# Performance work log

Measured on AMD Instinct MI355X. Metric: run time of the kernel, lower is better.

## Reference

```python
import jax, jax.numpy as jnp
import numpy as np
from jax import lax

KERNEL = 2
STACKS = 2
LAYERS = 10
DILATIONS = [2 ** l for _ in range(STACKS) for l in range(LAYERS)]  # 20 blocks
RECEPTIVE_FIELD = sum((KERNEL - 1) * d for d in DILATIONS)  # 2046


def setup_inputs() -> dict:
    key = jax.random.key(0)
    ks = jax.random.split(key, 8)
    B, L, C, NC = 8, 4096, 256, 256
    NB = len(DILATIONS)
    SK = L - RECEPTIVE_FIELD  # 2050

    def rn(k, shape, scale):
        return jax.random.normal(k, shape, jnp.float32) * scale

    return {
        "input_x": jax.random.normal(ks[0], (B, L, 1), jnp.float32),
        "causal_w": rn(ks[1], (1, C), 1.0),                 # 1x1 causal conv, in=1
        "causal_b": jnp.zeros((C,), jnp.float32),
        "dil_w": rn(ks[2], (NB, KERNEL, C, C), (KERNEL * C) ** -0.5),  # WIO per block
        "dil_b": jnp.zeros((NB, C), jnp.float32),
        "res_w": rn(ks[3], (NB, C, C), C ** -0.5),
        "res_b": jnp.zeros((NB, C), jnp.float32),
        "skip_w": rn(ks[4], (NB, C, C), C ** -0.5),
        "skip_b": jnp.zeros((NB, C), jnp.float32),
        "cls_conv_w": rn(ks[5], (C, C), C ** -0.5),
        "cls_conv_b": jnp.zeros((C,), jnp.float32),
        "dense_w": rn(ks[6], (SK * C, NC), (SK * C) ** -0.5),
        "dense_b": jnp.zeros((NC,), jnp.float32),
    }


def _conv1x1(x, w, b):
    # x: [B, T, Cin], w: [Cin, Cout]
    return jnp.einsum("btc,co->bto", x, w) + b


def _dilated_causal_conv(x, w, b, d):
    # keras 'causal' pad followed by slicing off the first (k-1)*d frames
    # is exactly a VALID dilated conv. x: [B,T,Cin], w: [K,Cin,Cout]
    y = lax.conv_general_dilated(
        x, w, window_strides=(1,), padding="VALID", rhs_dilation=(d,),
        dimension_numbers=("NWC", "WIO", "NWC"))
    return y + b


def reference(input_x, causal_w, causal_b, dil_w, dil_b, res_w, res_b,
              skip_w, skip_b, cls_conv_w, cls_conv_b, dense_w, dense_b):
    # initial causal conv (kernel_size=1 -> plain 1x1 conv)
    x = _conv1x1(input_x, causal_w, causal_b)  # [B, L, C]
    skip_size = x.shape[1] - RECEPTIVE_FIELD

    skips = []
    for i, d in enumerate(DILATIONS):
        h = _dilated_causal_conv(x, dil_w[i], dil_b[i], d)  # [B, T-(k-1)d, C]
        g = jnp.tanh(h) * jax.nn.sigmoid(h)                  # gated activation
        res = _conv1x1(g, res_w[i], res_b[i])
        x = res + g                                          # residual (same length)
        s = _conv1x1(g, skip_w[i], skip_b[i])[:, -skip_size:]
        skips.append(s)

    # classifier head: mean over blocks, relu, shared 1x1 conv twice, dense+softmax
    s = jnp.mean(jnp.stack(skips, 0), axis=0)  # [B, skip_size, C]
    s = jax.nn.relu(s)
    s = _conv1x1(s, cls_conv_w, cls_conv_b)
    s = jax.nn.relu(s)
    s = _conv1x1(s, cls_conv_w, cls_conv_b)    # same conv applied twice (shared weights)
    f = s.reshape(s.shape[0], -1)              # flatten [B, skip_size*C]
    logits = f @ dense_w + dense_b
    return jax.nn.softmax(logits, axis=-1)
```

## Files before the change

kernel.cpp:

```cpp
#include <hip/hip_runtime.h>

typedef __attribute__((ext_vector_type(8))) short short8;
typedef __attribute__((ext_vector_type(4))) float f32x4;
typedef unsigned int uint32;
typedef unsigned short u16;

#define CCH   256
#define BATCH 8
#define LFULL 4096
#define SKL   2050
#define BM    128
#define BN    128
#define LDK   72

#define GSTRIDE ((size_t)BATCH * LFULL * CCH)
#define XSTR    ((size_t)LFULL * CCH)
#define SSTR    ((size_t)SKL * CCH)
#define PSTR    ((size_t)BATCH * SKL * CCH)

__device__ const int TOUT[20] = {4095,4093,4089,4081,4065,4033,3969,3841,3585,3073,
                                 3072,3070,3066,3058,3042,3010,2946,2818,2562,2050};

__device__ __forceinline__ u16 f2b(float f) {
  uint32 u = __float_as_uint(f);
  u += 0x7fff + ((u >> 16) & 1);
  return (u16)(u >> 16);
}
__device__ __forceinline__ float gatef(float h) {
  float hc = fmaxf(h, -30.0f);
  float q = __expf(-hc);
  return (1.0f - q) * __builtin_amdgcn_rcpf(fmaf(q, q, 1.0f));
}
__device__ __forceinline__ void glds16(const void* g, void* l) {
  __builtin_amdgcn_global_load_lds(
      (const __attribute__((address_space(1))) void*)g,
      (__attribute__((address_space(3))) void*)l, 16, 0, 0);
}
__device__ __forceinline__ int xcd_swz(int orig, int nwg) {
  int xcd = orig & 7, idx = orig >> 3;
  int q = nwg >> 3, r = nwg & 7;
  int base = (xcd < r) ? xcd * (q + 1) : r * (q + 1) + (xcd - r) * q;
  return base + idx;
}

__global__ __launch_bounds__(256)
void compose_w(const float* __restrict__ res_w, const float* __restrict__ dil_w,
               u16* __restrict__ DWc) {
  __shared__ float As[32][256];
  int bx = blockIdx.x;
  int chunk = bx & 7, tap = (bx >> 3) & 1, bi = bx >> 4;
  int i = bi + 1;
  int co = threadIdx.x;
  int ci0 = chunk * 32;

  for (int idx = threadIdx.x; idx < 32 * 256; idx += 256) {
    int r = idx >> 8, m = idx & 255;
    float v = res_w[((size_t)(bi * 256 + ci0 + r)) * 256 + m];
    if (ci0 + r == m) v += 1.0f;
    As[r][m] = v;
  }
  __syncthreads();

  float acc[32];
  #pragma unroll
  for (int r = 0; r < 32; ++r) acc[r] = 0.0f;

  const float* Wb = dil_w + ((size_t)(i * 2 + tap) * 256) * 256 + co;
  for (int m4 = 0; m4 < 64; ++m4) {
    const float* wp = Wb + (size_t)m4 * 4 * 256;
    float w0 = wp[0], w1 = wp[256], w2 = wp[512], w3 = wp[768];
    #pragma unroll
    for (int r = 0; r < 32; ++r) {
      float4 a = *(const float4*)&As[r][m4 * 4];
      acc[r] = fmaf(a.x, w0, acc[r]);
      acc[r] = fmaf(a.y, w1, acc[r]);
      acc[r] = fmaf(a.z, w2, acc[r]);
      acc[r] = fmaf(a.w, w3, acc[r]);
    }
  }
  u16* op = DWc + ((size_t)(bi * 256 + co)) * 512 + tap * 256 + ci0;
  #pragma unroll
  for (int r = 0; r < 32; ++r) op[r] = f2b(acc[r]);
}

__global__ __launch_bounds__(256)
void compose_bias(const float* __restrict__ res_b, const float* __restrict__ dil_w,
                  const float* __restrict__ dil_b, float* __restrict__ Bc) {
  int bi = blockIdx.x, i = bi + 1, co = threadIdx.x;
  float acc = dil_b[(size_t)i * 256 + co];
  const float* W0 = dil_w + ((size_t)(i * 2 + 0) * 256) * 256;
  const float* W1 = dil_w + ((size_t)(i * 2 + 1) * 256) * 256;
  for (int m = 0; m < 256; ++m) {
    float rb = res_b[(size_t)bi * 256 + m];
    acc = fmaf(rb, W0[(size_t)m * 256 + co] + W1[(size_t)m * 256 + co], acc);
  }
  Bc[(size_t)bi * 256 + co] = acc;
}

__global__ __launch_bounds__(256)
void head0(const float* __restrict__ causal_w, const float* __restrict__ causal_b,
           const float* __restrict__ dil_w, const float* __restrict__ dil_b,
           float* __restrict__ U) {
  int co = threadIdx.x;
  float u0 = 0.f, u1 = 0.f, b0 = dil_b[co];
  for (int m = 0; m < 256; ++m) {
    float cwm = causal_w[m], cbm = causal_b[m];
    float w0 = dil_w[(size_t)m * 256 + co];
    float w1 = dil_w[(size_t)(256 + m) * 256 + co];
    u0 = fmaf(cwm, w0, u0);
    u1 = fmaf(cwm, w1, u1);
    b0 = fmaf(cbm, w0 + w1, b0);
  }
  U[co] = u0; U[256 + co] = u1; U[512 + co] = b0;
}

__global__ __launch_bounds__(256)
void g0_init(const float* __restrict__ in, const float* __restrict__ U,
             u16* __restrict__ G0) {
  int t = blockIdx.x, b = blockIdx.y, co = threadIdx.x;
  float x0 = in[(size_t)b * LFULL + t];
  float x1 = in[(size_t)b * LFULL + t + 1];
  float h = fmaf(x0, U[co], fmaf(x1, U[256 + co], U[512 + co]));
  G0[((size_t)b * LFULL + t) * CCH + co] = f2b(gatef(h));
}

__global__ __launch_bounds__(256)
void pack_skipT(const float* __restrict__ w, u16* __restrict__ o) {
  int e = blockIdx.x * 256 + threadIdx.x;
  int co = e & 255, ci = (e >> 8) & 255, i = e >> 16;
  o[(size_t)co * 5120 + i * 256 + ci] = f2b(w[e]);
}
__global__ __launch_bounds__(256)
void pack_cls(const float* __restrict__ w, u16* __restrict__ o) {
  int e = blockIdx.x * 256 + threadIdx.x;
  int co = e & 255, ci = e >> 8;
  o[(size_t)co * 256 + ci] = f2b(w[e]);
}
__global__ __launch_bounds__(256)
void sbsum_k(const float* __restrict__ sb, float* __restrict__ o) {
  int n = threadIdx.x;
  float s = 0.f;
  for (int i = 0; i < 20; ++i) s += sb[(size_t)i * 256 + n];
  o[n] = s;
}

__global__ __launch_bounds__(256)
void gatem(const u16* __restrict__ Ain, int d, int Tout, int ntile,
           const u16* __restrict__ Wt, const float* __restrict__ bias,
           u16* __restrict__ Gout) {
  __shared__ u16 As[2][BM * 64];
  __shared__ u16 Bs[2][BN * 64];

  const int tid = threadIdx.x;
  const int nwg = ntile * 16;
  const int wgid = xcd_swz(blockIdx.x, nwg);
  const int tx = wgid % ntile;
  const int rem = wgid / ntile;
  const int ny = rem & 1;
  const int bb = rem >> 1;

  const int t0 = tx * BM;
  const int n0 = ny * BN;
  const int lane = tid & 63, wv = tid >> 6;
  const int wm = wv >> 1, wn = wv & 1;
  const int fr = lane & 15, fq = lane >> 4;
  const int rl = lane >> 3;
  const int subx = ((lane & 7) ^ rl) * 8;
  const int rowb = wv * 32;

  const u16* Ab = Ain + (size_t)bb * XSTR;

  f32x4 acc[4][4];
  #pragma unroll
  for (int fn = 0; fn < 4; ++fn) {
    float4 bv = *(const float4*)&bias[n0 + wn * 64 + fn * 16 + fq * 4];
    #pragma unroll
    for (int fm = 0; fm < 4; ++fm) acc[fm][fn] = (f32x4){bv.x, bv.y, bv.z, bv.w};
  }

  auto STAGE = [&](int kt, int sel) {
    const int tap = kt >> 2, ks0 = (kt & 3) * 64;
    #pragma unroll
    for (int qq = 0; qq < 4; ++qq) {
      int rr = rowb + qq * 8 + rl;
      int t = t0 + rr;
      if (t > Tout - 1) t = Tout - 1;
      glds16(Ab + (size_t)(t + tap * d) * CCH + ks0 + subx,
             &As[sel][(rowb + qq * 8) * 64]);
      glds16(Wt + (size_t)(n0 + rr) * 512 + kt * 64 + subx,
             &Bs[sel][(rowb + qq * 8) * 64]);
    }
  };

  STAGE(0, 0);
  for (int kt = 0; kt < 8; ++kt) {
    const int cur = kt & 1;
    if (kt < 7) {
      STAGE(kt + 1, cur ^ 1);
      asm volatile("s_waitcnt vmcnt(8)" ::: "memory");
    } else {
      asm volatile("s_waitcnt vmcnt(0)" ::: "memory");
    }
    __builtin_amdgcn_s_barrier();
    __builtin_amdgcn_sched_barrier(0);

    #pragma unroll
    for (int ks = 0; ks < 2; ++ks) {
      short8 af[4], bfr[4];
      #pragma unroll
      for (int fm = 0; fm < 4; ++fm) {
        int row = wm * 64 + fm * 16 + fr;
        af[fm] = *(const short8*)&As[cur][row * 64 + ((ks * 4 + fq) ^ (row & 7)) * 8];
      }
      #pragma unroll
      for (int fn = 0; fn < 4; ++fn) {
        int row = wn * 64 + fn * 16 + fr;
        bfr[fn] = *(const short8*)&Bs[cur][row * 64 + ((ks * 4 + fq) ^ (row & 7)) * 8];
      }
      #pragma unroll
      for (int fm = 0; fm < 4; ++fm)
        #pragma unroll
        for (int fn = 0; fn < 4; ++fn)
          acc[fm][fn] = __builtin_amdgcn_mfma_f32_16x16x32_bf16(
              bfr[fn], af[fm], acc[fm][fn], 0, 0, 0);
    }
    __builtin_amdgcn_s_barrier();
  }

  u16* Ob = Gout + (size_t)bb * XSTR;
  #pragma unroll
  for (int fm = 0; fm < 4; ++fm) {
    int t = t0 + wm * 64 + fm * 16 + fr;
    if (t >= Tout) continue;
    #pragma unroll
    for (int fn = 0; fn < 4; ++fn) {
      int c0 = n0 + wn * 64 + fn * 16 + fq * 4;
      f32x4 a = acc[fm][fn];
      uint32 p0 = (uint32)f2b(gatef(a[0])) | ((uint32)f2b(gatef(a[1])) << 16);
      uint32 p1 = (uint32)f2b(gatef(a[2])) | ((uint32)f2b(gatef(a[3])) << 16);
      uint2 pk; pk.x = p0; pk.y = p1;
      *(uint2*)(Ob + (size_t)t * CCH + c0) = pk;
    }
  }
}

__global__ __launch_bounds__(256)
void skipm(const u16* __restrict__ Gh, const u16* __restrict__ SWT,
           float* __restrict__ P) {
  __shared__ u16 As[2][BM * 64];
  __shared__ u16 Bs[2][BN * 64];

  const int tid = threadIdx.x;
  const int nwg = 17 * 2 * 32;
  const int wgid = xcd_swz(blockIdx.x, nwg);
  const int tx = wgid % 17;
  const int rem = wgid / 17;
  const int ny = rem & 1;
  const int zz = rem >> 1;
  const int b = zz >> 2, j = zz & 3;

  const int t0 = tx * BM;
  const int n0 = ny * BN;
  const int lane = tid & 63, wv = tid >> 6;
  const int wm = wv >> 1, wn = wv & 1;
  const int fr = lane & 15, fq = lane >> 4;
  const int rl = lane >> 3;
  const int subx = ((lane & 7) ^ rl) * 8;
  const int rowb = wv * 32;

  f32x4 acc[4][4];
  #pragma unroll
  for (int fm = 0; fm < 4; ++fm)
    #pragma unroll
    for (int fn = 0; fn < 4; ++fn) acc[fm][fn] = (f32x4){0.f, 0.f, 0.f, 0.f};

  auto STAGE = [&](int kt, int sel) {
    const int i = j * 5 + (kt >> 2);
    const int toff = TOUT[i] - SKL;
    const int ks0 = (kt & 3) * 64;
    const u16* Gi = Gh + (size_t)i * GSTRIDE + (size_t)b * XSTR;
    #pragma unroll
    for (int qq = 0; qq < 4; ++qq) {
      int rr = rowb + qq * 8 + rl;
      int t = t0 + rr;
      if (t > SKL - 1) t = SKL - 1;
      glds16(Gi + (size_t)(toff + t) * CCH + ks0 + subx,
             &As[sel][(rowb + qq * 8) * 64]);
      glds16(SWT + (size_t)(n0 + rr) * 5120 + i * 256 + ks0 + subx,
             &Bs[sel][(rowb + qq * 8) * 64]);
    }
  };

  STAGE(0, 0);
  for (int kt = 0; kt < 20; ++kt) {
    const int cur = kt & 1;
    if (kt < 19) {
      STAGE(kt + 1, cur ^ 1);
      asm volatile("s_waitcnt vmcnt(8)" ::: "memory");
    } else {
      asm volatile("s_waitcnt vmcnt(0)" ::: "memory");
    }
    __builtin_amdgcn_s_barrier();
    __builtin_amdgcn_sched_barrier(0);

    #pragma unroll
    for (int ks = 0; ks < 2; ++ks) {
      short8 af[4], bfr[4];
      #pragma unroll
      for (int fm = 0; fm < 4; ++fm) {
        int row = wm * 64 + fm * 16 + fr;
        af[fm] = *(const short8*)&As[cur][row * 64 + ((ks * 4 + fq) ^ (row & 7)) * 8];
      }
      #pragma unroll
      for (int fn = 0; fn < 4; ++fn) {
        int row = wn * 64 + fn * 16 + fr;
        bfr[fn] = *(const short8*)&Bs[cur][row * 64 + ((ks * 4 + fq) ^ (row & 7)) * 8];
      }
      #pragma unroll
      for (int fm = 0; fm < 4; ++fm)
        #pragma unroll
        for (int fn = 0; fn < 4; ++fn)
          acc[fm][fn] = __builtin_amdgcn_mfma_f32_16x16x32_bf16(
              bfr[fn], af[fm], acc[fm][fn], 0, 0, 0);
    }
    __builtin_amdgcn_s_barrier();
  }

  float* Pj = P + (size_t)j * PSTR + (size_t)b * SSTR;
  #pragma unroll
  for (int fm = 0; fm < 4; ++fm) {
    int t = t0 + wm * 64 + fm * 16 + fr;
    if (t >= SKL) continue;
    #pragma unroll
    for (int fn = 0; fn < 4; ++fn) {
      int c0 = n0 + wn * 64 + fn * 16 + fq * 4;
      f32x4 a = acc[fm][fn];
      float4 o = {a[0], a[1], a[2], a[3]};
      *(float4*)(Pj + (size_t)t * CCH + c0) = o;
    }
  }
}

enum { MODE_CLS1 = 1, MODE_CLS2 = 2 };

template <int MODE>
__global__ __launch_bounds__(256)
void convm(const void* __restrict__ Ainv, long a_bstride,
           const u16* __restrict__ Wt, const float* __restrict__ bias,
           const float* __restrict__ extra,
           void* __restrict__ Out1, long out_bstride, int Tout) {
  __shared__ u16 As[BM * LDK];
  __shared__ u16 Bs[BN * LDK];

  const int tid = threadIdx.x;
  const int bb  = blockIdx.z;
  const int t0  = blockIdx.x * BM;
  const int n0  = blockIdx.y * BN;
  const int lane = tid & 63, wv = tid >> 6;
  const int wm = wv >> 1, wn = wv & 1;
  const int fr = lane & 15, fq = lane >> 4;

  f32x4 acc[4][4];
  #pragma unroll
  for (int fn = 0; fn < 4; ++fn) {
    float bv = bias[n0 + wn * 64 + fn * 16 + fr];
    #pragma unroll
    for (int fm = 0; fm < 4; ++fm) acc[fm][fn] = (f32x4){bv, bv, bv, bv};
  }

  for (int kt = 0; kt < 4; ++kt) {
    for (int idx = tid; idx < 1024; idx += 256) {
      int r = idx >> 3, c8 = idx & 7;
      int t = t0 + r; if (t > Tout - 1) t = Tout - 1;
      uint4 v;
      if constexpr (MODE == MODE_CLS1) {
        const float* p0 = (const float*)Ainv + (size_t)bb * a_bstride +
                          (size_t)t * CCH + kt * 64 + c8 * 8;
        float4 s0 = *(const float4*)p0;
        float4 s1 = *(const float4*)(p0 + 4);
        #pragma unroll
        for (int jj = 1; jj < 4; ++jj) {
          const float* pj = p0 + (size_t)jj * PSTR;
          float4 a0 = *(const float4*)pj;
          float4 a1 = *(const float4*)(pj + 4);
          s0.x += a0.x; s0.y += a0.y; s0.z += a0.z; s0.w += a0.w;
          s1.x += a1.x; s1.y += a1.y; s1.z += a1.z; s1.w += a1.w;
        }
        float4 e0 = *(const float4*)&extra[kt * 64 + c8 * 8];
        float4 e1 = *(const float4*)&extra[kt * 64 + c8 * 8 + 4];
        u16 tmp[8];
        tmp[0] = f2b(fmaxf((s0.x + e0.x) * 0.05f, 0.f));
        tmp[1] = f2b(fmaxf((s0.y + e0.y) * 0.05f, 0.f));
        tmp[2] = f2b(fmaxf((s0.z + e0.z) * 0.05f, 0.f));
        tmp[3] = f2b(fmaxf((s0.w + e0.w) * 0.05f, 0.f));
        tmp[4] = f2b(fmaxf((s1.x + e1.x) * 0.05f, 0.f));
        tmp[5] = f2b(fmaxf((s1.y + e1.y) * 0.05f, 0.f));
        tmp[6] = f2b(fmaxf((s1.z + e1.z) * 0.05f, 0.f));
        tmp[7] = f2b(fmaxf((s1.w + e1.w) * 0.05f, 0.f));
        v = *(uint4*)tmp;
      } else {
        const u16* sp = (const u16*)Ainv + (size_t)bb * a_bstride +
                        (size_t)t * CCH + kt * 64 + c8 * 8;
        uint4 raw = *(const uint4*)sp;
        u16 tmp[8];
        *(uint4*)tmp = raw;
        #pragma unroll
        for (int jj = 0; jj < 8; ++jj) tmp[jj] = (tmp[jj] & 0x8000) ? (u16)0 : tmp[jj];
        v = *(uint4*)tmp;
      }
      *(uint4*)&As[r * LDK + c8 * 8] = v;
    }
    for (int idx = tid; idx < 1024; idx += 256) {
      int r = idx >> 3, c8 = idx & 7;
      const u16* sp = Wt + (size_t)(n0 + r) * 256 + kt * 64 + c8 * 8;
      *(uint4*)&Bs[r * LDK + c8 * 8] = *(const uint4*)sp;
    }
    __syncthreads();

    #pragma unroll
    for (int ks = 0; ks < 2; ++ks) {
      short8 af[4], bfr[4];
      #pragma unroll
      for (int fm = 0; fm < 4; ++fm)
        af[fm] = *(const short8*)&As[(wm * 64 + fm * 16 + fr) * LDK + ks * 32 + fq * 8];
      #pragma unroll
      for (int fn = 0; fn < 4; ++fn)
        bfr[fn] = *(const short8*)&Bs[(wn * 64 + fn * 16 + fr) * LDK + ks * 32 + fq * 8];
      #pragma unroll
      for (int fm = 0; fm < 4; ++fm)
        #pragma unroll
        for (int fn = 0; fn < 4; ++fn)
          acc[fm][fn] = __builtin_amdgcn_mfma_f32_16x16x32_bf16(
              af[fm], bfr[fn], acc[fm][fn], 0, 0, 0);
    }
    __syncthreads();
  }

  #pragma unroll
  for (int fm = 0; fm < 4; ++fm) {
    int rbase = t0 + wm * 64 + fm * 16 + fq * 4;
    #pragma unroll
    for (int r = 0; r < 4; ++r) {
      int t = rbase + r;
      if (t >= Tout) continue;
      #pragma unroll
      for (int fn = 0; fn < 4; ++fn) {
        int c = n0 + wn * 64 + fn * 16 + fr;
        float a = acc[fm][fn][r];
        size_t oix = (size_t)bb * out_bstride + (size_t)t * CCH + c;
        if constexpr (MODE == MODE_CLS1) {
          ((u16*)Out1)[oix] = f2b(a);
        } else {
          ((float*)Out1)[oix] = a;
        }
      }
    }
  }
}

__global__ __launch_bounds__(256)
void dense_partial(const float* __restrict__ f, const float* __restrict__ W,
                   float* __restrict__ part) {
  int tstep = blockIdx.x;
  int n = threadIdx.x;
  __shared__ float fs[BATCH][CCH];
  for (int idx = threadIdx.x; idx < BATCH * CCH; idx += 256) {
    int b = idx >> 8, c = idx & 255;
    fs[b][c] = f[((size_t)b * SKL + tstep) * CCH + c];
  }
  __syncthreads();
  float acc[BATCH] = {0.f, 0.f, 0.f, 0.f, 0.f, 0.f, 0.f, 0.f};
  const float* Wr = W + (size_t)tstep * CCH * CCH;
  for (int ci = 0; ci < CCH; ++ci) {
    float w = Wr[(size_t)ci * CCH + n];
    #pragma unroll
    for (int b = 0; b < BATCH; ++b) acc[b] = fmaf(fs[b][ci], w, acc[b]);
  }
  #pragma unroll
  for (int b = 0; b < BATCH; ++b)
    part[((size_t)tstep * BATCH + b) * CCH + n] = acc[b];
}

__global__ __launch_bounds__(256)
void reduce_part(const float* __restrict__ part, float* __restrict__ part2) {
  int chunk = blockIdx.x, b = blockIdx.y, n = threadIdx.x;
  int c0 = chunk * 33;
  int c1 = c0 + 33; if (c1 > SKL) c1 = SKL;
  float s = 0.f;
  for (int c = c0; c < c1; ++c) s += part[((size_t)c * BATCH + b) * CCH + n];
  part2[((size_t)b * 64 + chunk) * CCH + n] = s;
}

__global__ __launch_bounds__(256)
void softmax_k(const float* __restrict__ part2, const float* __restrict__ db,
               float* __restrict__ out) {
  int b = blockIdx.x, n = threadIdx.x;
  float s = db[n];
  for (int ch = 0; ch < 64; ++ch) s += part2[((size_t)b * 64 + ch) * CCH + n];

  __shared__ float r4[4];
  __shared__ float mglob, sglob;
  int wid = n >> 6, lane = n & 63;

  float m = s;
  #pragma unroll
  for (int off = 1; off < 64; off <<= 1) m = fmaxf(m, __shfl_xor(m, off));
  if (lane == 0) r4[wid] = m;
  __syncthreads();
  if (n == 0) mglob = fmaxf(fmaxf(r4[0], r4[1]), fmaxf(r4[2], r4[3]));
  __syncthreads();

  float e = expf(s - mglob);
  float se = e;
  #pragma unroll
  for (int off = 1; off < 64; off <<= 1) se += __shfl_xor(se, off);
  if (lane == 0) r4[wid] = se;
  __syncthreads();
  if (n == 0) sglob = r4[0] + r4[1] + r4[2] + r4[3];
  __syncthreads();

  out[(size_t)b * CCH + n] = e / sglob;
}

extern "C" void kernel_launch(void* const* d_in, const int* in_sizes, int n_in,
                              void* d_out, int out_size, void* d_ws, size_t ws_size,
                              hipStream_t stream) {
  const float* input_x  = (const float*)d_in[0];
  const float* causal_w = (const float*)d_in[1];
  const float* causal_b = (const float*)d_in[2];
  const float* dil_w    = (const float*)d_in[3];
  const float* dil_b    = (const float*)d_in[4];
  const float* res_w    = (const float*)d_in[5];
  const float* res_b    = (const float*)d_in[6];
  const float* skip_w   = (const float*)d_in[7];
  const float* skip_b   = (const float*)d_in[8];
  const float* cls_w    = (const float*)d_in[9];
  const float* cls_b    = (const float*)d_in[10];
  const float* dense_w  = (const float*)d_in[11];
  const float* dense_b  = (const float*)d_in[12];
  float* out = (float*)d_out;

  char* p = (char*)d_ws;
  u16*   Gh    = (u16*)p;   p += GSTRIDE * 20 * 2;
  float* P     = (float*)p; p += PSTR * 4 * 4;
  u16*   S1    = (u16*)p;   p += (size_t)BATCH * SKL * CCH * 2;
  float* S2    = (float*)p; p += (size_t)BATCH * SKL * CCH * 4;
  float* PART  = (float*)p; p += (size_t)SKL * BATCH * CCH * 4;
  float* PART2 = (float*)p; p += (size_t)BATCH * 64 * CCH * 4;
  u16*   DWc   = (u16*)p;   p += (size_t)19 * 256 * 512 * 2;
  float* Bc    = (float*)p; p += (size_t)19 * 256 * 4;
  u16*   SWT   = (u16*)p;   p += (size_t)256 * 5120 * 2;
  u16*   CW    = (u16*)p;   p += (size_t)256 * 256 * 2;
  float* U     = (float*)p; p += (size_t)768 * 4;
  float* SBS   = (float*)p; p += (size_t)256 * 4;

  static const int dil[20] = {1, 2, 4, 8, 16, 32, 64, 128, 256, 512,
                              1, 2, 4, 8, 16, 32, 64, 128, 256, 512};
  static const int tout_h[20] = {4095,4093,4089,4081,4065,4033,3969,3841,3585,3073,
                                 3072,3070,3066,3058,3042,3010,2946,2818,2562,2050};
  dim3 blk(256);
  const int stile = (SKL + BM - 1) / BM;

  compose_w   <<<dim3(19 * 2 * 8), blk, 0, stream>>>(res_w, dil_w, DWc);
  compose_bias<<<dim3(19), blk, 0, stream>>>(res_b, dil_w, dil_b, Bc);
  head0       <<<dim3(1), blk, 0, stream>>>(causal_w, causal_b, dil_w, dil_b, U);
  pack_skipT  <<<dim3(20 * 256), blk, 0, stream>>>(skip_w, SWT);
  pack_cls    <<<dim3(256), blk, 0, stream>>>(cls_w, CW);
  sbsum_k     <<<dim3(1), blk, 0, stream>>>(skip_b, SBS);

  g0_init<<<dim3(4095, BATCH), blk, 0, stream>>>(input_x, U, Gh);

  for (int i = 1; i < 20; ++i) {
    int Tout = tout_h[i];
    int ntile = (Tout + BM - 1) / BM;
    gatem<<<dim3(ntile * 16), blk, 0, stream>>>(
        Gh + (size_t)(i - 1) * GSTRIDE, dil[i], Tout, ntile,
        DWc + (size_t)(i - 1) * 256 * 512, Bc + (size_t)(i - 1) * 256,
        Gh + (size_t)i * GSTRIDE);
  }

  skipm<<<dim3(17 * 2 * 32), blk, 0, stream>>>(Gh, SWT, P);

  convm<MODE_CLS1><<<dim3(stile, 2, BATCH), blk, 0, stream>>>(
      P, (long)SSTR, CW, cls_b, SBS, S1, (long)SSTR, SKL);
  convm<MODE_CLS2><<<dim3(stile, 2, BATCH), blk, 0, stream>>>(
      S1, (long)SSTR, CW, cls_b, nullptr, S2, (long)SSTR, SKL);

  dense_partial<<<dim3(SKL), blk, 0, stream>>>(S2, dense_w, PART);
  reduce_part<<<dim3(64, BATCH), blk, 0, stream>>>(PART, PART2);
  softmax_k<<<dim3(BATCH), blk, 0, stream>>>(PART2, dense_b, out);
}
```

Baseline: 703.8 us.

## Load weight fragments directly into registers instead of staging through LDS

In both the gated dilated-conv GEMM and the skip GEMM, the B (weight) operand is no longer staged in shared memory. Each wave loads its weight fragments from global memory straight into double-buffered registers, and the k-loop is fully unrolled. This halves LDS use and removes LDS reads for B, which may raise occupancy. The cost is extra VGPRs, redundant global weight loads across the wave-rows that share B (relying on cache), and a waitcnt count that must match the new load count.

```diff
diff --git a/kernel.cpp b/kernel.cpp
--- a/kernel.cpp
+++ b/kernel.cpp
@@ -149,7 +149,6 @@
            const u16* __restrict__ Wt, const float* __restrict__ bias,
            u16* __restrict__ Gout) {
   __shared__ u16 As[2][BM * 64];
-  __shared__ u16 Bs[2][BN * 64];
 
   const int tid = threadIdx.x;
   const int nwg = ntile * 16;
@@ -169,6 +168,7 @@
   const int rowb = wv * 32;
 
   const u16* Ab = Ain + (size_t)bb * XSTR;
+  const u16* Wb = Wt + (size_t)(n0 + wn * 64 + fr) * 512 + fq * 8;
 
   f32x4 acc[4][4];
   #pragma unroll
@@ -178,7 +178,7 @@
     for (int fm = 0; fm < 4; ++fm) acc[fm][fn] = (f32x4){bv.x, bv.y, bv.z, bv.w};
   }
 
-  auto STAGE = [&](int kt, int sel) {
+  auto STAGE_A = [&](int kt, int sel) {
     const int tap = kt >> 2, ks0 = (kt & 3) * 64;
     #pragma unroll
     for (int qq = 0; qq < 4; ++qq) {
@@ -187,17 +187,29 @@
       if (t > Tout - 1) t = Tout - 1;
       glds16(Ab + (size_t)(t + tap * d) * CCH + ks0 + subx,
              &As[sel][(rowb + qq * 8) * 64]);
-      glds16(Wt + (size_t)(n0 + rr) * 512 + kt * 64 + subx,
-             &Bs[sel][(rowb + qq * 8) * 64]);
     }
   };
-
-  STAGE(0, 0);
+  auto LOADB = [&](int kt, short8* br) {
+    #pragma unroll
+    for (int fn = 0; fn < 4; ++fn)
+      #pragma unroll
+      for (int ks = 0; ks < 2; ++ks)
+        br[fn * 2 + ks] = *(const short8*)(Wb + fn * 16 * 512 + kt * 64 + ks * 32);
+  };
+
+  short8 b0r[8], b1r[8];
+  STAGE_A(0, 0);
+  LOADB(0, b0r);
+
+  #pragma unroll
   for (int kt = 0; kt < 8; ++kt) {
     const int cur = kt & 1;
+    short8* bc = cur ? b1r : b0r;
+    short8* bn = cur ? b0r : b1r;
     if (kt < 7) {
-      STAGE(kt + 1, cur ^ 1);
-      asm volatile("s_waitcnt vmcnt(8)" ::: "memory");
+      STAGE_A(kt + 1, cur ^ 1);
+      LOADB(kt + 1, bn);
+      asm volatile("s_waitcnt vmcnt(12)" ::: "memory");
     } else {
       asm volatile("s_waitcnt vmcnt(0)" ::: "memory");
     }
@@ -206,23 +218,18 @@
 
     #pragma unroll
     for (int ks = 0; ks < 2; ++ks) {
-      short8 af[4], bfr[4];
+      short8 af[4];
       #pragma unroll
       for (int fm = 0; fm < 4; ++fm) {
         int row = wm * 64 + fm * 16 + fr;
         af[fm] = *(const short8*)&As[cur][row * 64 + ((ks * 4 + fq) ^ (row & 7)) * 8];
       }
       #pragma unroll
-      for (int fn = 0; fn < 4; ++fn) {
-        int row = wn * 64 + fn * 16 + fr;
-        bfr[fn] = *(const short8*)&Bs[cur][row * 64 + ((ks * 4 + fq) ^ (row & 7)) * 8];
-      }
-      #pragma unroll
       for (int fm = 0; fm < 4; ++fm)
         #pragma unroll
         for (int fn = 0; fn < 4; ++fn)
           acc[fm][fn] = __builtin_amdgcn_mfma_f32_16x16x32_bf16(
-              bfr[fn], af[fm], acc[fm][fn], 0, 0, 0);
+              bc[fn * 2 + ks], af[fm], acc[fm][fn], 0, 0, 0);
     }
     __builtin_amdgcn_s_barrier();
   }
@@ -248,7 +255,6 @@
 void skipm(const u16* __restrict__ Gh, const u16* __restrict__ SWT,
            float* __restrict__ P) {
   __shared__ u16 As[2][BM * 64];
-  __shared__ u16 Bs[2][BN * 64];
 
   const int tid = threadIdx.x;
   const int nwg = 17 * 2 * 32;
@@ -268,17 +274,20 @@
   const int subx = ((lane & 7) ^ rl) * 8;
   const int rowb = wv * 32;
 
+  const u16* Wb = SWT + (size_t)(n0 + wn * 64 + fr) * 5120 + j * 5 * 256 + fq * 8;
+  const u16* Gb = Gh + (size_t)b * XSTR;
+
   f32x4 acc[4][4];
   #pragma unroll
   for (int fm = 0; fm < 4; ++fm)
     #pragma unroll
     for (int fn = 0; fn < 4; ++fn) acc[fm][fn] = (f32x4){0.f, 0.f, 0.f, 0.f};
 
-  auto STAGE = [&](int kt, int sel) {
+  auto STAGE_A = [&](int kt, int sel) {
     const int i = j * 5 + (kt >> 2);
     const int toff = TOUT[i] - SKL;
     const int ks0 = (kt & 3) * 64;
-    const u16* Gi = Gh + (size_t)i * GSTRIDE + (size_t)b * XSTR;
+    const u16* Gi = Gb + (size_t)i * GSTRIDE;
     #pragma unroll
     for (int qq = 0; qq < 4; ++qq) {
       int rr = rowb + qq * 8 + rl;
@@ -286,17 +295,30 @@
       if (t > SKL - 1) t = SKL - 1;
       glds16(Gi + (size_t)(toff + t) * CCH + ks0 + subx,
              &As[sel][(rowb + qq * 8) * 64]);
-      glds16(SWT + (size_t)(n0 + rr) * 5120 + i * 256 + ks0 + subx,
-             &Bs[sel][(rowb + qq * 8) * 64]);
     }
   };
-
-  STAGE(0, 0);
+  auto LOADB = [&](int kt, short8* br) {
+    const int koff = (kt >> 2) * 256 + (kt & 3) * 64;
+    #pragma unroll
+    for (int fn = 0; fn < 4; ++fn)
+      #pragma unroll
+      for (int ks = 0; ks < 2; ++ks)
+        br[fn * 2 + ks] = *(const short8*)(Wb + fn * 16 * 5120 + koff + ks * 32);
+  };
+
+  short8 b0r[8], b1r[8];
+  STAGE_A(0, 0);
+  LOADB(0, b0r);
+
+  #pragma unroll
   for (int kt = 0; kt < 20; ++kt) {
     const int cur = kt & 1;
+    short8* bc = cur ? b1r : b0r;
+    short8* bn = cur ? b0r : b1r;
     if (kt < 19) {
-      STAGE(kt + 1, cur ^ 1);
-      asm volatile("s_waitcnt vmcnt(8)" ::: "memory");
+      STAGE_A(kt + 1, cur ^ 1);
+      LOADB(kt + 1, bn);
+      asm volatile("s_waitcnt vmcnt(12)" ::: "memory");
     } else {
       asm volatile("s_waitcnt vmcnt(0)" ::: "memory");
     }
@@ -305,23 +327,18 @@
 
     #pragma unroll
     for (int ks = 0; ks < 2; ++ks) {
-      short8 af[4], bfr[4];
+      short8 af[4];
       #pragma unroll
       for (int fm = 0; fm < 4; ++fm) {
         int row = wm * 64 + fm * 16 + fr;
         af[fm] = *(const short8*)&As[cur][row * 64 + ((ks * 4 + fq) ^ (row & 7)) * 8];
       }
       #pragma unroll
-      for (int fn = 0; fn < 4; ++fn) {
-        int row = wn * 64 + fn * 16 + fr;
-        bfr[fn] = *(const short8*)&Bs[cur][row * 64 + ((ks * 4 + fq) ^ (row & 7)) * 8];
-      }
-      #pragma unroll
       for (int fm = 0; fm < 4; ++fm)
         #pragma unroll
         for (int fn = 0; fn < 4; ++fn)
           acc[fm][fn] = __builtin_amdgcn_mfma_f32_16x16x32_bf16(
-              bfr[fn], af[fm], acc[fm][fn], 0, 0, 0);
+              bc[fn * 2 + ks], af[fm], acc[fm][fn], 0, 0, 0);
     }
     __builtin_amdgcn_s_barrier();
   }
```

After: 886.7 us. 26.0% more time.

## Fuse g0_init and 19 gated-conv launches into one persistent kernel with grid barrier

Applied to the files above, without the earlier changes.

Replaces the initial gating kernel and the 19 per-layer gatem launches with a single persistent kernel of 512 workgroups. The workgroups loop over tiles and synchronise between layers through an atomic-counter grid barrier. The aim is to remove per-launch overhead and the tail idle time between dependent layer launches. In exchange it depends on all 512 blocks being co-resident (launch_bounds(256,2)) to avoid deadlock, and it adds barrier spin cost and possibly worse load balance on the grid-stride tile loops.

```diff
diff --git a/kernel.cpp b/kernel.cpp
--- a/kernel.cpp
+++ b/kernel.cpp
@@ -12,14 +12,17 @@
 #define BM    128
 #define BN    128
 #define LDK   72
+#define NBLK  512
 
 #define GSTRIDE ((size_t)BATCH * LFULL * CCH)
 #define XSTR    ((size_t)LFULL * CCH)
 #define SSTR    ((size_t)SKL * CCH)
 #define PSTR    ((size_t)BATCH * SKL * CCH)
 
-__device__ const int TOUT[20] = {4095,4093,4089,4081,4065,4033,3969,3841,3585,3073,
-                                 3072,3070,3066,3058,3042,3010,2946,2818,2562,2050};
+__device__ const int TOUTD[20] = {4095,4093,4089,4081,4065,4033,3969,3841,3585,3073,
+                                  3072,3070,3066,3058,3042,3010,2946,2818,2562,2050};
+__device__ const int DILD[20]  = {1,2,4,8,16,32,64,128,256,512,
+                                  1,2,4,8,16,32,64,128,256,512};
 
 __device__ __forceinline__ u16 f2b(float f) {
   uint32 u = __float_as_uint(f);
@@ -115,16 +118,6 @@
 }
 
 __global__ __launch_bounds__(256)
-void g0_init(const float* __restrict__ in, const float* __restrict__ U,
-             u16* __restrict__ G0) {
-  int t = blockIdx.x, b = blockIdx.y, co = threadIdx.x;
-  float x0 = in[(size_t)b * LFULL + t];
-  float x1 = in[(size_t)b * LFULL + t + 1];
-  float h = fmaf(x0, U[co], fmaf(x1, U[256 + co], U[512 + co]));
-  G0[((size_t)b * LFULL + t) * CCH + co] = f2b(gatef(h));
-}
-
-__global__ __launch_bounds__(256)
 void pack_skipT(const float* __restrict__ w, u16* __restrict__ o) {
   int e = blockIdx.x * 256 + threadIdx.x;
   int co = e & 255, ci = (e >> 8) & 255, i = e >> 16;
@@ -144,20 +137,152 @@
   o[n] = s;
 }
 
-__global__ __launch_bounds__(256)
-void gatem(const u16* __restrict__ Ain, int d, int Tout, int ntile,
-           const u16* __restrict__ Wt, const float* __restrict__ bias,
-           u16* __restrict__ Gout) {
+__global__ __launch_bounds__(256, 2)
+void chain(const float* __restrict__ in, const float* __restrict__ U,
+           const u16* __restrict__ DWc, const float* __restrict__ Bc,
+           u16* __restrict__ Gh, uint32* __restrict__ bar) {
   __shared__ u16 As[2][BM * 64];
   __shared__ u16 Bs[2][BN * 64];
 
   const int tid = threadIdx.x;
-  const int nwg = ntile * 16;
+  const int lane = tid & 63, wv = tid >> 6;
+  const int wm = wv >> 1, wn = wv & 1;
+  const int fr = lane & 15, fq = lane >> 4;
+  const int rl = lane >> 3;
+  const int subx = ((lane & 7) ^ rl) * 8;
+  const int rowb = wv * 32;
+
+  {
+    float u0 = U[tid], u1 = U[256 + tid], b0 = U[512 + tid];
+    for (int row = blockIdx.x; row < BATCH * 4095; row += NBLK) {
+      int b = row / 4095, t = row - b * 4095;
+      float x0 = in[(size_t)b * LFULL + t];
+      float x1 = in[(size_t)b * LFULL + t + 1];
+      float h = fmaf(x0, u0, fmaf(x1, u1, b0));
+      Gh[((size_t)b * LFULL + t) * CCH + tid] = f2b(gatef(h));
+    }
+  }
+
+  for (int i = 1; i < 20; ++i) {
+    __syncthreads();
+    if (tid == 0) {
+      __threadfence();
+      atomicAdd(bar, 1u);
+      uint32 target = (uint32)NBLK * (uint32)i;
+      while (atomicAdd(bar, 0u) < target) __builtin_amdgcn_s_sleep(4);
+    }
+    __syncthreads();
+    __threadfence();
+
+    const int d = DILD[i];
+    const int Tout = TOUTD[i];
+    const int ntile = (Tout + BM - 1) / BM;
+    const int nwg = ntile * 16;
+    const u16* Ain = Gh + (size_t)(i - 1) * GSTRIDE;
+    u16* Gout = Gh + (size_t)i * GSTRIDE;
+    const u16* Wt = DWc + (size_t)(i - 1) * 256 * 512;
+    const float* bias = Bc + (size_t)(i - 1) * 256;
+
+    for (int w = blockIdx.x; w < nwg; w += NBLK) {
+      const int wgid = xcd_swz(w, nwg);
+      const int tx = wgid % ntile;
+      const int rem = wgid / ntile;
+      const int ny = rem & 1;
+      const int bb = rem >> 1;
+      const int t0 = tx * BM;
+      const int n0 = ny * BN;
+      const u16* Ab = Ain + (size_t)bb * XSTR;
+
+      f32x4 acc[4][4];
+      #pragma unroll
+      for (int fn = 0; fn < 4; ++fn) {
+        float4 bv = *(const float4*)&bias[n0 + wn * 64 + fn * 16 + fq * 4];
+        #pragma unroll
+        for (int fm = 0; fm < 4; ++fm) acc[fm][fn] = (f32x4){bv.x, bv.y, bv.z, bv.w};
+      }
+
+      auto STAGE = [&](int kt, int sel) {
+        const int tap = kt >> 2, ks0 = (kt & 3) * 64;
+        #pragma unroll
+        for (int qq = 0; qq < 4; ++qq) {
+          int rr = rowb + qq * 8 + rl;
+          int t = t0 + rr;
+          if (t > Tout - 1) t = Tout - 1;
+          glds16(Ab + (size_t)(t + tap * d) * CCH + ks0 + subx,
+                 &As[sel][(rowb + qq * 8) * 64]);
+          glds16(Wt + (size_t)(n0 + rr) * 512 + kt * 64 + subx,
+                 &Bs[sel][(rowb + qq * 8) * 64]);
+        }
+      };
+
+      STAGE(0, 0);
+      for (int kt = 0; kt < 8; ++kt) {
+        const int cur = kt & 1;
+        if (kt < 7) {
+          STAGE(kt + 1, cur ^ 1);
+          asm volatile("s_waitcnt vmcnt(8)" ::: "memory");
+        } else {
+          asm volatile("s_waitcnt vmcnt(0)" ::: "memory");
+        }
+        __builtin_amdgcn_s_barrier();
+        __builtin_amdgcn_sched_barrier(0);
+
+        #pragma unroll
+        for (int ks = 0; ks < 2; ++ks) {
+          short8 af[4], bfr[4];
+          #pragma unroll
+          for (int fm = 0; fm < 4; ++fm) {
+            int row = wm * 64 + fm * 16 + fr;
+            af[fm] = *(const short8*)&As[cur][row * 64 + ((ks * 4 + fq) ^ (row & 7)) * 8];
+          }
+          #pragma unroll
+          for (int fn = 0; fn < 4; ++fn) {
+            int row = wn * 64 + fn * 16 + fr;
+            bfr[fn] = *(const short8*)&Bs[cur][row * 64 + ((ks * 4 + fq) ^ (row & 7)) * 8];
+          }
+          #pragma unroll
+          for (int fm = 0; fm < 4; ++fm)
+            #pragma unroll
+            for (int fn = 0; fn < 4; ++fn)
+              acc[fm][fn] = __builtin_amdgcn_mfma_f32_16x16x32_bf16(
+                  bfr[fn], af[fm], acc[fm][fn], 0, 0, 0);
+        }
+        __builtin_amdgcn_s_barrier();
+      }
+
+      u16* Ob = Gout + (size_t)bb * XSTR;
+      #pragma unroll
+      for (int fm = 0; fm < 4; ++fm) {
+        int t = t0 + wm * 64 + fm * 16 + fr;
+        if (t >= Tout) continue;
+        #pragma unroll
+        for (int fn = 0; fn < 4; ++fn) {
+          int c0 = n0 + wn * 64 + fn * 16 + fq * 4;
+          f32x4 a = acc[fm][fn];
+          uint32 p0 = (uint32)f2b(gatef(a[0])) | ((uint32)f2b(gatef(a[1])) << 16);
+          uint32 p1 = (uint32)f2b(gatef(a[2])) | ((uint32)f2b(gatef(a[3])) << 16);
+          uint2 pk; pk.x = p0; pk.y = p1;
+          *(uint2*)(Ob + (size_t)t * CCH + c0) = pk;
+        }
+      }
+    }
+  }
+}
+
+__global__ __launch_bounds__(256)
+void skipm(const u16* __restrict__ Gh, const u16* __restrict__ SWT,
+           float* __restrict__ P) {
+  __shared__ u16 As[2][BM * 64];
+  __shared__ u16 Bs[2][BN * 64];
+
+  const int tid = threadIdx.x;
+  const int nwg = 17 * 2 * 32;
   const int wgid = xcd_swz(blockIdx.x, nwg);
-  const int tx = wgid % ntile;
-  const int rem = wgid / ntile;
+  const int tx = wgid % 17;
+  const int rem = wgid / 17;
   const int ny = rem & 1;
-  const int bb = rem >> 1;
+  const int zz = rem >> 1;
+  const int b = zz >> 2, j = zz & 3;
 
   const int t0 = tx * BM;
   const int n0 = ny * BN;
@@ -168,106 +293,6 @@
   const int subx = ((lane & 7) ^ rl) * 8;
   const int rowb = wv * 32;
 
-  const u16* Ab = Ain + (size_t)bb * XSTR;
-
-  f32x4 acc[4][4];
-  #pragma unroll
-  for (int fn = 0; fn < 4; ++fn) {
-    float4 bv = *(const float4*)&bias[n0 + wn * 64 + fn * 16 + fq * 4];
-    #pragma unroll
-    for (int fm = 0; fm < 4; ++fm) acc[fm][fn] = (f32x4){bv.x, bv.y, bv.z, bv.w};
-  }
-
-  auto STAGE = [&](int kt, int sel) {
-    const int tap = kt >> 2, ks0 = (kt & 3) * 64;
-    #pragma unroll
-    for (int qq = 0; qq < 4; ++qq) {
-      int rr = rowb + qq * 8 + rl;
-      int t = t0 + rr;
-      if (t > Tout - 1) t = Tout - 1;
-      glds16(Ab + (size_t)(t + tap * d) * CCH + ks0 + subx,
-             &As[sel][(rowb + qq * 8) * 64]);
-      glds16(Wt + (size_t)(n0 + rr) * 512 + kt * 64 + subx,
-             &Bs[sel][(rowb + qq * 8) * 64]);
-    }
-  };
-
-  STAGE(0, 0);
-  for (int kt = 0; kt < 8; ++kt) {
-    const int cur = kt & 1;
-    if (kt < 7) {
-      STAGE(kt + 1, cur ^ 1);
-      asm volatile("s_waitcnt vmcnt(8)" ::: "memory");
-    } else {
-      asm volatile("s_waitcnt vmcnt(0)" ::: "memory");
-    }
-    __builtin_amdgcn_s_barrier();
-    __builtin_amdgcn_sched_barrier(0);
-
-    #pragma unroll
-    for (int ks = 0; ks < 2; ++ks) {
-      short8 af[4], bfr[4];
-      #pragma unroll
-      for (int fm = 0; fm < 4; ++fm) {
-        int row = wm * 64 + fm * 16 + fr;
-        af[fm] = *(const short8*)&As[cur][row * 64 + ((ks * 4 + fq) ^ (row & 7)) * 8];
-      }
-      #pragma unroll
-      for (int fn = 0; fn < 4; ++fn) {
-        int row = wn * 64 + fn * 16 + fr;
-        bfr[fn] = *(const short8*)&Bs[cur][row * 64 + ((ks * 4 + fq) ^ (row & 7)) * 8];
-      }
-      #pragma unroll
-      for (int fm = 0; fm < 4; ++fm)
-        #pragma unroll
-        for (int fn = 0; fn < 4; ++fn)
-          acc[fm][fn] = __builtin_amdgcn_mfma_f32_16x16x32_bf16(
-              bfr[fn], af[fm], acc[fm][fn], 0, 0, 0);
-    }
-    __builtin_amdgcn_s_barrier();
-  }
-
-  u16* Ob = Gout + (size_t)bb * XSTR;
-  #pragma unroll
-  for (int fm = 0; fm < 4; ++fm) {
-    int t = t0 + wm * 64 + fm * 16 + fr;
-    if (t >= Tout) continue;
-    #pragma unroll
-    for (int fn = 0; fn < 4; ++fn) {
-      int c0 = n0 + wn * 64 + fn * 16 + fq * 4;
-      f32x4 a = acc[fm][fn];
-      uint32 p0 = (uint32)f2b(gatef(a[0])) | ((uint32)f2b(gatef(a[1])) << 16);
-      uint32 p1 = (uint32)f2b(gatef(a[2])) | ((uint32)f2b(gatef(a[3])) << 16);
-      uint2 pk; pk.x = p0; pk.y = p1;
-      *(uint2*)(Ob + (size_t)t * CCH + c0) = pk;
-    }
-  }
-}
-
-__global__ __launch_bounds__(256)
-void skipm(const u16* __restrict__ Gh, const u16* __restrict__ SWT,
-           float* __restrict__ P) {
-  __shared__ u16 As[2][BM * 64];
-  __shared__ u16 Bs[2][BN * 64];
-
-  const int tid = threadIdx.x;
-  const int nwg = 17 * 2 * 32;
-  const int wgid = xcd_swz(blockIdx.x, nwg);
-  const int tx = wgid % 17;
-  const int rem = wgid / 17;
-  const int ny = rem & 1;
-  const int zz = rem >> 1;
-  const int b = zz >> 2, j = zz & 3;
-
-  const int t0 = tx * BM;
-  const int n0 = ny * BN;
-  const int lane = tid & 63, wv = tid >> 6;
-  const int wm = wv >> 1, wn = wv & 1;
-  const int fr = lane & 15, fq = lane >> 4;
-  const int rl = lane >> 3;
-  const int subx = ((lane & 7) ^ rl) * 8;
-  const int rowb = wv * 32;
-
   f32x4 acc[4][4];
   #pragma unroll
   for (int fm = 0; fm < 4; ++fm)
@@ -276,7 +301,7 @@
 
   auto STAGE = [&](int kt, int sel) {
     const int i = j * 5 + (kt >> 2);
-    const int toff = TOUT[i] - SKL;
+    const int toff = TOUTD[i] - SKL;
     const int ks0 = (kt & 3) * 64;
     const u16* Gi = Gh + (size_t)i * GSTRIDE + (size_t)b * XSTR;
     #pragma unroll
@@ -553,11 +578,8 @@
   u16*   CW    = (u16*)p;   p += (size_t)256 * 256 * 2;
   float* U     = (float*)p; p += (size_t)768 * 4;
   float* SBS   = (float*)p; p += (size_t)256 * 4;
-
-  static const int dil[20] = {1, 2, 4, 8, 16, 32, 64, 128, 256, 512,
-                              1, 2, 4, 8, 16, 32, 64, 128, 256, 512};
-  static const int tout_h[20] = {4095,4093,4089,4081,4065,4033,3969,3841,3585,3073,
-                                 3072,3070,3066,3058,3042,3010,2946,2818,2562,2050};
+  uint32* BAR  = (uint32*)p; p += 256;
+
   dim3 blk(256);
   const int stile = (SKL + BM - 1) / BM;
 
@@ -568,16 +590,9 @@
   pack_cls    <<<dim3(256), blk, 0, stream>>>(cls_w, CW);
   sbsum_k     <<<dim3(1), blk, 0, stream>>>(skip_b, SBS);
 
-  g0_init<<<dim3(4095, BATCH), blk, 0, stream>>>(input_x, U, Gh);
-
-  for (int i = 1; i < 20; ++i) {
-    int Tout = tout_h[i];
-    int ntile = (Tout + BM - 1) / BM;
-    gatem<<<dim3(ntile * 16), blk, 0, stream>>>(
-        Gh + (size_t)(i - 1) * GSTRIDE, dil[i], Tout, ntile,
-        DWc + (size_t)(i - 1) * 256 * 512, Bc + (size_t)(i - 1) * 256,
-        Gh + (size_t)i * GSTRIDE);
-  }
+  hipMemsetAsync(BAR, 0, 4, stream);
+
+  chain<<<dim3(NBLK), blk, 0, stream>>>(input_x, U, DWc, Bc, Gh, BAR);
 
   skipm<<<dim3(17 * 2 * 32), blk, 0, stream>>>(Gh, SWT, P);
 
```

New measurement: 2.129 ms. +202.5%, slower.
